# Kernel tuning notes

Hardware: AMD Instinct MI355X
Metric: run time of the kernel (lower is better)

Reference implementation:

```python
import jax, jax.numpy as jnp
import numpy as np

B, T, C = 2, 2048, 1024
H, HD = 16, 64
M = 256  # per memory bank
K_CANON = 4


def setup_inputs() -> dict:
    key = jax.random.key(0)
    ks = jax.random.split(key, 10)
    s = 0.02
    return {
        "x": jax.random.normal(ks[0], (B, T, C), jnp.float32),
        "fwd_mem": jax.random.normal(ks[1], (B, M, C), jnp.float32),
        "rev_mem": jax.random.normal(ks[2], (B, M, C), jnp.float32),
        "Wq": jax.random.normal(ks[3], (C, C), jnp.float32) * s,
        "Wk": jax.random.normal(ks[4], (C, C), jnp.float32) * s,
        "Wv": jax.random.normal(ks[5], (C, C), jnp.float32) * s,
        "Wo": jax.random.normal(ks[6], (C, C), jnp.float32) * s,
        "gate_w": jax.random.normal(ks[7], (H, C), jnp.float32) * s,
        "gate_b": jnp.zeros((H,), jnp.float32),
        "canon_w": jax.random.normal(ks[8], (C, 1, K_CANON), jnp.float32) * s,
        "canon_bias": jax.random.normal(ks[9], (C,), jnp.float32) * s,
    }


def _canon_conv(y, canon_w, canon_bias):
    # causal depthwise conv1d with residual; torch weight [C,1,K] -> WIO kernel [K,1,C]
    kern = jnp.transpose(canon_w, (2, 1, 0))
    y_pad = jnp.pad(y, ((0, 0), (K_CANON - 1, 0), (0, 0)))
    conv = jax.lax.conv_general_dilated(
        y_pad, kern, window_strides=(1,), padding='VALID',
        dimension_numbers=('NWC', 'WIO', 'NWC'), feature_group_count=C)
    return y + conv + canon_bias


def reference(x, fwd_mem, rev_mem, Wq, Wk, Wv, Wo, gate_w, gate_b, canon_w, canon_bias):
    Bn, Tn, Cn = x.shape
    scale = 1.0 / np.sqrt(HD)

    q = x @ Wq.T  # [B,T,C]
    k = x @ Wk.T
    v = x @ Wv.T
    # memory integration: project memories with same k/v proj, concat on seq dim
    k = jnp.concatenate([k, fwd_mem @ Wk.T, rev_mem @ Wk.T], axis=1)  # [B,S,C]
    v = jnp.concatenate([v, fwd_mem @ Wv.T, rev_mem @ Wv.T], axis=1)
    S = k.shape[1]
    mem_len = S - Tn

    def heads(t):
        return t.reshape(Bn, -1, H, HD).transpose(0, 2, 1, 3)  # [B,h,S,hd]

    qh, kh, vh = heads(q), heads(k), heads(v)
    scores = jnp.einsum('bhtd,bhsd->bhts', qh, kh) * scale  # [B,h,T,S]
    # causal mask over the first T key columns; memory columns fully visible
    causal = jnp.triu(jnp.ones((Tn, Tn), bool), k=1)
    full_mask = jnp.pad(causal, ((0, 0), (0, mem_len)))  # [T,S]
    scores = jnp.where(full_mask[None, None], -jnp.inf, scores)
    w = jax.nn.softmax(scores, axis=-1)

    # split chunk vs memory, gate memory contribution per head
    w_chunk, w_mem = w[..., :Tn], w[..., Tn:]
    v_chunk, v_mem = vh[:, :, :Tn], vh[:, :, Tn:]
    Y_chunk = jnp.einsum('bhts,bhsd->bhtd', w_chunk, v_chunk)
    Y_mem = jnp.einsum('bhtm,bhmd->bhtd', w_mem, v_mem)
    g = jax.nn.sigmoid(q @ gate_w.T + gate_b)  # [B,T,h]
    g = g.transpose(0, 2, 1)[..., None]  # [B,h,T,1]
    Y = Y_chunk + g * Y_mem

    attn_out = Y.transpose(0, 2, 1, 3).reshape(Bn, Tn, Cn)
    attn_out = _canon_conv(attn_out, canon_w, canon_bias)
    return attn_out @ Wo.T
```

## Files before the change

### kernel.cpp

```cpp
#include <hip/hip_runtime.h>
#include <hip/hip_bf16.h>
#include <cstdint>


typedef __bf16 bf16x8_t __attribute__((ext_vector_type(8)));
typedef __bf16 bf16x4_t __attribute__((ext_vector_type(4)));
typedef float f32x4_t __attribute__((ext_vector_type(4)));

__device__ __forceinline__ f32x4_t mfma16(bf16x8_t a, bf16x8_t b, f32x4_t c) {
    return __builtin_amdgcn_mfma_f32_16x16x32_bf16(a, b, c, 0, 0, 0);
}

__device__ __forceinline__ void gl2lds16(const void* g, void* l) {
    __builtin_amdgcn_global_load_lds(
        (__attribute__((address_space(1))) uint32_t*)(uintptr_t)g,
        (__attribute__((address_space(3))) uint32_t*)l, 16, 0, 0);
}

#define OFF_X   0
#define OFF_FWD 4194304
#define OFF_REV 4718592
#define OFF_WQ  5242880
#define OFF_WK  6291456
#define OFF_WV  7340032
#define OFF_WO  8388608
#define OFF_GW  9437184
#define OFF_GB  9453568
#define OFF_CW  9453584
#define OFF_CB  9457680
#define N_TOT   9458704

__global__ __launch_bounds__(256) void conv_all_kernel(
    const void* p0, const void* p1, const void* p2, const void* p3,
    const void* p4, const void* p5, const void* p6, const void* p7,
    const void* p8, const void* p9, const void* p10,
    __hip_bfloat16* __restrict__ arena)
{
    const int i = (blockIdx.x * 256 + threadIdx.x) * 4;
    if (i >= N_TOT) return;
    const void* src; int off;
    if      (i < OFF_FWD) { src = p0;  off = OFF_X;   }
    else if (i < OFF_REV) { src = p1;  off = OFF_FWD; }
    else if (i < OFF_WQ)  { src = p2;  off = OFF_REV; }
    else if (i < OFF_WK)  { src = p3;  off = OFF_WQ;  }
    else if (i < OFF_WV)  { src = p4;  off = OFF_WK;  }
    else if (i < OFF_WO)  { src = p5;  off = OFF_WV;  }
    else if (i < OFF_GW)  { src = p6;  off = OFF_WO;  }
    else if (i < OFF_GB)  { src = p7;  off = OFF_GW;  }
    else if (i < OFF_CW)  { src = p8;  off = OFF_GB;  }
    else if (i < OFF_CB)  { src = p9;  off = OFF_CW;  }
    else                  { src = p10; off = OFF_CB;  }
    const int j = i - off;
    const float4 f = *(const float4*)((const float*)src + j);
    arena[i + 0] = __float2bfloat16(f.x);
    arena[i + 1] = __float2bfloat16(f.y);
    arena[i + 2] = __float2bfloat16(f.z);
    arena[i + 3] = __float2bfloat16(f.w);
}

__device__ __forceinline__ void gemm_core(
    const __hip_bfloat16* __restrict__ A, const __hip_bfloat16* __restrict__ B,
    void* __restrict__ C, int ldc, int f32o, int arow0, int brow0,
    __hip_bfloat16* As, __hip_bfloat16* Bs)
{
    const int tid  = threadIdx.x;
    const int lane = tid & 63;
    const int wid  = tid >> 6;
    const int q4   = lane >> 4;
    const int c16  = lane & 15;
    const int wm   = (wid >> 1) * 64;
    const int wn   = (wid & 1) * 64;
    const int c0 = tid;
    const int c1 = tid + 256;
    const __hip_bfloat16* gA0 = A + (size_t)(arow0 + (c0 >> 2)) * 1024 + ((c0 & 3) << 3);
    const __hip_bfloat16* gA1 = A + (size_t)(arow0 + (c1 >> 2)) * 1024 + ((c1 & 3) << 3);
    const __hip_bfloat16* gB0 = B + (size_t)(brow0 + (c0 >> 2)) * 1024 + ((c0 & 3) << 3);
    const __hip_bfloat16* gB1 = B + (size_t)(brow0 + (c1 >> 2)) * 1024 + ((c1 & 3) << 3);

    f32x4_t acc[4][4];
#pragma unroll
    for (int i = 0; i < 4; ++i)
#pragma unroll
        for (int j = 0; j < 4; ++j)
#pragma unroll
            for (int r = 0; r < 4; ++r) acc[i][j][r] = 0.0f;

    gl2lds16(gA0, As + c0 * 8);
    gl2lds16(gA1, As + c1 * 8);
    gl2lds16(gB0, Bs + c0 * 8);
    gl2lds16(gB1, Bs + c1 * 8);

    for (int it = 0; it < 32; ++it) {
        __hip_bfloat16* curA = As + (it & 1) * 4096;
        __hip_bfloat16* curB = Bs + (it & 1) * 4096;
        __syncthreads();
        if (it < 31) {
            const int nk = (it + 1) * 32;
            __hip_bfloat16* nA = As + ((it + 1) & 1) * 4096;
            __hip_bfloat16* nB = Bs + ((it + 1) & 1) * 4096;
            gl2lds16(gA0 + nk, nA + c0 * 8);
            gl2lds16(gA1 + nk, nA + c1 * 8);
            gl2lds16(gB0 + nk, nB + c0 * 8);
            gl2lds16(gB1 + nk, nB + c1 * 8);
        }
        bf16x8_t af[4], bfr[4];
#pragma unroll
        for (int i = 0; i < 4; ++i)
            af[i] = *(const bf16x8_t*)&curA[(wm + i * 16 + c16) * 32 + q4 * 8];
#pragma unroll
        for (int j = 0; j < 4; ++j)
            bfr[j] = *(const bf16x8_t*)&curB[(wn + j * 16 + c16) * 32 + q4 * 8];
#pragma unroll
        for (int i = 0; i < 4; ++i)
#pragma unroll
            for (int j = 0; j < 4; ++j)
                acc[i][j] = mfma16(af[i], bfr[j], acc[i][j]);
    }
#pragma unroll
    for (int i = 0; i < 4; ++i) {
        const int mg = arow0 + wm + i * 16 + q4 * 4;
#pragma unroll
        for (int j = 0; j < 4; ++j) {
            const int ng = brow0 + wn + j * 16 + c16;
#pragma unroll
            for (int r = 0; r < 4; ++r) {
                const size_t idx = (size_t)(mg + r) * ldc + ng;
                if (f32o) ((float*)C)[idx] = acc[i][j][r];
                else ((__hip_bfloat16*)C)[idx] = __float2bfloat16(acc[i][j][r]);
            }
        }
    }
}

__global__ __launch_bounds__(256) void qkv_kernel(
    const __hip_bfloat16* __restrict__ x, const __hip_bfloat16* __restrict__ Wqk,
    const __hip_bfloat16* __restrict__ Wv,
    __hip_bfloat16* __restrict__ QK, __hip_bfloat16* __restrict__ Vt)
{
    __shared__ __align__(16) __hip_bfloat16 As[2 * 128 * 32];
    __shared__ __align__(16) __hip_bfloat16 Bs[2 * 128 * 32];
    int id = blockIdx.x;
    if (id < 640)
        gemm_core(x, Wqk, QK, 2048, 0, (id >> 4) * 128, (id & 15) * 128, As, Bs);
    else {
        id -= 640;
        gemm_core(Wv, x, Vt, 5120, 0, (id & 7) * 128, (id >> 3) * 128, As, Bs);
    }
}

__global__ __launch_bounds__(256) void gemm_bt_kernel(
    const __hip_bfloat16* __restrict__ A, const __hip_bfloat16* __restrict__ B,
    void* __restrict__ C, int ldc, int f32o)
{
    __shared__ __align__(16) __hip_bfloat16 As[2 * 128 * 32];
    __shared__ __align__(16) __hip_bfloat16 Bs[2 * 128 * 32];
    gemm_core(A, B, C, ldc, f32o, blockIdx.x * 128, blockIdx.y * 128, As, Bs);
}

__global__ __launch_bounds__(64) void gate_kernel(
    const __hip_bfloat16* __restrict__ QK, const __hip_bfloat16* __restrict__ gw,
    const __hip_bfloat16* __restrict__ gb, float* __restrict__ G)
{
    const int base = blockIdx.x * 16;
    const int lane = threadIdx.x;
    const int q4   = lane >> 4;
    const int c16  = lane & 15;
    f32x4_t acc = {0.0f, 0.0f, 0.0f, 0.0f};
    const __hip_bfloat16* qrow = QK + (size_t)(base + c16) * 2048 + q4 * 8;
    const __hip_bfloat16* wrow = gw + (size_t)c16 * 1024 + q4 * 8;
#pragma unroll
    for (int kk = 0; kk < 32; ++kk) {
        const bf16x8_t a = *(const bf16x8_t*)(qrow + kk * 32);
        const bf16x8_t w = *(const bf16x8_t*)(wrow + kk * 32);
        acc = mfma16(a, w, acc);
    }
    const float bias = __bfloat162float(gb[c16]);
#pragma unroll
    for (int r = 0; r < 4; ++r) {
        const int row = base + q4 * 4 + r;
        G[(size_t)row * 16 + c16] = 1.0f / (1.0f + __expf(-(acc[r] + bias)));
    }
}

__global__ __launch_bounds__(256, 4) void attn_kernel(
    const __hip_bfloat16* __restrict__ QK,
    const __hip_bfloat16* __restrict__ Vt,
    const float* __restrict__ G, __hip_bfloat16* __restrict__ Y)
{
    __shared__ __align__(16) __hip_bfloat16 Ks[2][64 * 64];
    __shared__ __align__(16) __hip_bfloat16 Vs[64 * 64];
    __shared__ __align__(16) __hip_bfloat16 Plds[4][16 * 64];
    const int flat = blockIdx.x;
    const int bh   = flat & 31;
    const int tIdx = 31 - (flat >> 5);
    const int b    = bh >> 4;
    const int h    = bh & 15;
    const int tid  = threadIdx.x;
    const int wid  = tid >> 6;
    const int lane = tid & 63;
    const int q4   = lane >> 4;
    const int c16  = lane & 15;
    const int rowbase = tIdx * 64 + wid * 16;

    const __hip_bfloat16* qrow = QK + (size_t)(b * 2048 + rowbase + c16) * 2048 + h * 64;
    const bf16x8_t qa0 = *(const bf16x8_t*)(qrow + q4 * 8);
    const bf16x8_t qa1 = *(const bf16x8_t*)(qrow + 32 + q4 * 8);

    float rs[4], gate[4];
    f32x4_t acc[4];
#pragma unroll
    for (int fp = 0; fp < 4; ++fp)
#pragma unroll
        for (int r = 0; r < 4; ++r) acc[fp][r] = 0.0f;
#pragma unroll
    for (int r = 0; r < 4; ++r) {
        rs[r] = 0.0f;
        gate[r] = G[(size_t)(b * 2048 + rowbase + q4 * 4 + r) * 16 + h];
    }

    const int nCausal = tIdx + 1;
    const int nTiles  = nCausal + 8;
    auto kvRow = [&](int tile) -> int {
        if (tile < nCausal) return b * 2048 + tile * 64;
        const int mi = (tile - nCausal) * 64;
        return (mi < 256) ? 4096 + b * 256 + mi : 4608 + b * 256 + (mi - 256);
    };

    const int srow0 = tid >> 3,         sch0 = (tid & 7) ^ (srow0 & 7);
    const int srow1 = (tid + 256) >> 3, sch1 = (tid & 7) ^ (srow1 & 7);
    const int sw0 = (q4 ^ (c16 & 7)) * 8;
    const int sw1 = ((q4 + 4) ^ (c16 & 7)) * 8;
    const __hip_bfloat16* Kbase = QK + 1024 + h * 64;

    {
        const int vr0 = kvRow(0);
        gl2lds16(Kbase + (size_t)(vr0 + srow0) * 2048 + sch0 * 8, &Ks[0][tid * 8]);
        gl2lds16(Kbase + (size_t)(vr0 + srow1) * 2048 + sch1 * 8, &Ks[0][(tid + 256) * 8]);
    }

    const float SCL = 0.18033688f;

    for (int tile = 0; tile < nTiles; ++tile) {
        const int cur = tile & 1;
        const int vr  = kvRow(tile);
        __syncthreads();
        gl2lds16(Vt + (size_t)(h * 64 + srow0) * 5120 + vr + sch0 * 8, &Vs[tid * 8]);
        gl2lds16(Vt + (size_t)(h * 64 + srow1) * 5120 + vr + sch1 * 8, &Vs[(tid + 256) * 8]);
        if (tile + 1 < nTiles) {
            const int nr = kvRow(tile + 1);
            gl2lds16(Kbase + (size_t)(nr + srow0) * 2048 + sch0 * 8, &Ks[cur ^ 1][tid * 8]);
            gl2lds16(Kbase + (size_t)(nr + srow1) * 2048 + sch1 * 8, &Ks[cur ^ 1][(tid + 256) * 8]);
        }
        const bool isMem  = (tile >= nCausal);
        const bool isDiag = (tile == nCausal - 1);
        bf16x8_t kb0[4], kb1[4];
#pragma unroll
        for (int f = 0; f < 4; ++f) {
            kb0[f] = *(const bf16x8_t*)&Ks[cur][(f * 16 + c16) * 64 + sw0];
            kb1[f] = *(const bf16x8_t*)&Ks[cur][(f * 16 + c16) * 64 + sw1];
        }
        f32x4_t sc[4];
#pragma unroll
        for (int f = 0; f < 4; ++f) {
            f32x4_t z = {0.0f, 0.0f, 0.0f, 0.0f};
            z = mfma16(qa0, kb0[f], z);
            z = mfma16(qa1, kb1[f], z);
            sc[f] = z;
        }
#pragma unroll
        for (int f = 0; f < 4; ++f)
#pragma unroll
            for (int r = 0; r < 4; ++r) {
                float p = __builtin_amdgcn_exp2f(sc[f][r] * SCL);
                if (isDiag) {
                    const int sg = f * 16 + c16;
                    if (sg > wid * 16 + q4 * 4 + r) p = 0.0f;
                }
                rs[r] += p;
                if (isMem) p *= gate[r];
                const int prow = q4 * 4 + r;
                const int pcol = f * 16 + c16;
                Plds[wid][prow * 64 + (((pcol >> 3) ^ (prow & 7)) << 3) + (pcol & 7)] =
                    __float2bfloat16(p);
            }
        __syncthreads();
        bf16x8_t vb0[4], vb1[4];
#pragma unroll
        for (int f = 0; f < 4; ++f) {
            vb0[f] = *(const bf16x8_t*)&Vs[(f * 16 + c16) * 64 + sw0];
            vb1[f] = *(const bf16x8_t*)&Vs[(f * 16 + c16) * 64 + sw1];
        }
        const bf16x8_t pa0 = *(const bf16x8_t*)&Plds[wid][c16 * 64 + sw0];
        const bf16x8_t pa1 = *(const bf16x8_t*)&Plds[wid][c16 * 64 + sw1];
#pragma unroll
        for (int fp = 0; fp < 4; ++fp) {
            acc[fp] = mfma16(pa0, vb0[fp], acc[fp]);
            acc[fp] = mfma16(pa1, vb1[fp], acc[fp]);
        }
    }
#pragma unroll
    for (int m = 1; m <= 8; m <<= 1)
#pragma unroll
        for (int r = 0; r < 4; ++r) rs[r] += __shfl_xor(rs[r], m, 64);
    float inv[4];
#pragma unroll
    for (int r = 0; r < 4; ++r) inv[r] = 1.0f / rs[r];
#pragma unroll
    for (int fp = 0; fp < 4; ++fp)
#pragma unroll
        for (int r = 0; r < 4; ++r) {
            const int tg = rowbase + q4 * 4 + r;
            Y[(size_t)(b * 2048 + tg) * 1024 + h * 64 + fp * 16 + c16] =
                __float2bfloat16(acc[fp][r] * inv[r]);
        }
}

__global__ __launch_bounds__(256) void canon_kernel(
    const __hip_bfloat16* __restrict__ Yin, const __hip_bfloat16* __restrict__ cw,
    const __hip_bfloat16* __restrict__ cb, __hip_bfloat16* __restrict__ Yout)
{
    const int idx = (blockIdx.x * 256 + threadIdx.x) * 4;
    const int c = idx & 1023;
    const int t = (idx >> 10) & 2047;
    const bf16x4_t y0 = *(const bf16x4_t*)(Yin + idx);
    const bf16x4_t bb = *(const bf16x4_t*)(cb + c);
    float a[4];
#pragma unroll
    for (int i = 0; i < 4; ++i) a[i] = (float)y0[i] + (float)bb[i];
    const bf16x8_t w01 = *(const bf16x8_t*)(cw + c * 4);
    const bf16x8_t w23 = *(const bf16x8_t*)(cw + c * 4 + 8);
#pragma unroll
    for (int j = 0; j < 4; ++j) {
        if (t - 3 + j >= 0) {
            const bf16x4_t yj = *(const bf16x4_t*)(Yin + idx + (j - 3) * 1024);
            a[0] += (float)yj[0] * (float)w01[j];
            a[1] += (float)yj[1] * (float)w01[4 + j];
            a[2] += (float)yj[2] * (float)w23[j];
            a[3] += (float)yj[3] * (float)w23[4 + j];
        }
    }
    bf16x4_t o;
#pragma unroll
    for (int i = 0; i < 4; ++i) o[i] = (__bf16)a[i];
    *(bf16x4_t*)(Yout + idx) = o;
}

extern "C" void kernel_launch(void* const* d_in, const int* in_sizes, int n_in,
                              void* d_out, int out_size, void* d_ws, size_t ws_size,
                              hipStream_t stream)
{
    char* ws = (char*)d_ws;
    const size_t MB = 1ull << 20;
    if (ws_size < 50 * MB) return;

    __hip_bfloat16* arena = (__hip_bfloat16*)ws;
    __hip_bfloat16* QK    = (__hip_bfloat16*)(ws + 19 * MB);
    __hip_bfloat16* Vt    = (__hip_bfloat16*)(ws + 39 * MB);
    float*          G     = (float*)(ws + 49 * MB);
    __hip_bfloat16* Y1    = (__hip_bfloat16*)ws;
    __hip_bfloat16* Y2    = QK;

    const dim3 blk(256);
    conv_all_kernel<<<dim3((N_TOT / 4 + 255) / 256), blk, 0, stream>>>(
        d_in[0], d_in[1], d_in[2], d_in[3], d_in[4], d_in[5], d_in[6],
        d_in[7], d_in[8], d_in[9], d_in[10], arena);

    const __hip_bfloat16* xB  = arena + OFF_X;
    const __hip_bfloat16* WqB = arena + OFF_WQ;
    const __hip_bfloat16* WvB = arena + OFF_WV;
    const __hip_bfloat16* WoB = arena + OFF_WO;

    qkv_kernel<<<dim3(960), blk, 0, stream>>>(xB, WqB, WvB, QK, Vt);
    gate_kernel<<<dim3(256), dim3(64), 0, stream>>>(QK, arena + OFF_GW, arena + OFF_GB, G);
    attn_kernel<<<dim3(1024), blk, 0, stream>>>(QK, Vt, G, Y1);
    canon_kernel<<<dim3(4096), blk, 0, stream>>>(Y1, arena + OFF_CW, arena + OFF_CB, Y2);
    gemm_bt_kernel<<<dim3(32, 8), blk, 0, stream>>>(Y2, WoB, d_out, 1024, 1);
}
```

Measured before the change: 240.0 us.

## Skip Q projection for memory rows, MFMA row sums, prioritize MFMA waves

```diff
diff --git a/kernel.cpp b/kernel.cpp
--- a/kernel.cpp
+++ b/kernel.cpp
@@ -140,10 +140,13 @@
     __shared__ __align__(16) __hip_bfloat16 As[2 * 128 * 32];
     __shared__ __align__(16) __hip_bfloat16 Bs[2 * 128 * 32];
     int id = blockIdx.x;
-    if (id < 640)
+    if (id < 512)
         gemm_core(x, Wqk, QK, 2048, 0, (id >> 4) * 128, (id & 15) * 128, As, Bs);
-    else {
-        id -= 640;
+    else if (id < 576) {
+        id -= 512;
+        gemm_core(x, Wqk, QK, 2048, 0, (32 + (id >> 3)) * 128, (8 + (id & 7)) * 128, As, Bs);
+    } else {
+        id -= 576;
         gemm_core(Wv, x, Vt, 5120, 0, (id & 7) * 128, (id >> 3) * 128, As, Bs);
     }
 }
@@ -206,17 +209,21 @@
     const bf16x8_t qa0 = *(const bf16x8_t*)(qrow + q4 * 8);
     const bf16x8_t qa1 = *(const bf16x8_t*)(qrow + 32 + q4 * 8);
 
-    float rs[4], gate[4];
+    bf16x8_t ones;
+#pragma unroll
+    for (int i = 0; i < 8; ++i) ones[i] = (__bf16)1.0f;
+
+    float gate[4];
     f32x4_t acc[4];
+    f32x4_t rsC = {0.0f, 0.0f, 0.0f, 0.0f};
+    f32x4_t rsM = {0.0f, 0.0f, 0.0f, 0.0f};
 #pragma unroll
     for (int fp = 0; fp < 4; ++fp)
 #pragma unroll
         for (int r = 0; r < 4; ++r) acc[fp][r] = 0.0f;
 #pragma unroll
-    for (int r = 0; r < 4; ++r) {
-        rs[r] = 0.0f;
+    for (int r = 0; r < 4; ++r)
         gate[r] = G[(size_t)(b * 2048 + rowbase + q4 * 4 + r) * 16 + h];
-    }
 
     const int nCausal = tIdx + 1;
     const int nTiles  = nCausal + 8;
@@ -260,6 +267,7 @@
             kb1[f] = *(const bf16x8_t*)&Ks[cur][(f * 16 + c16) * 64 + sw1];
         }
         f32x4_t sc[4];
+        __builtin_amdgcn_s_setprio(1);
 #pragma unroll
         for (int f = 0; f < 4; ++f) {
             f32x4_t z = {0.0f, 0.0f, 0.0f, 0.0f};
@@ -267,6 +275,7 @@
             z = mfma16(qa1, kb1[f], z);
             sc[f] = z;
         }
+        __builtin_amdgcn_s_setprio(0);
 #pragma unroll
         for (int f = 0; f < 4; ++f)
 #pragma unroll
@@ -276,7 +285,6 @@
                     const int sg = f * 16 + c16;
                     if (sg > wid * 16 + q4 * 4 + r) p = 0.0f;
                 }
-                rs[r] += p;
                 if (isMem) p *= gate[r];
                 const int prow = q4 * 4 + r;
                 const int pcol = f * 16 + c16;
@@ -292,19 +300,26 @@
         }
         const bf16x8_t pa0 = *(const bf16x8_t*)&Plds[wid][c16 * 64 + sw0];
         const bf16x8_t pa1 = *(const bf16x8_t*)&Plds[wid][c16 * 64 + sw1];
+        __builtin_amdgcn_s_setprio(1);
+        if (isMem) {
+            rsM = mfma16(pa0, ones, rsM);
+            rsM = mfma16(pa1, ones, rsM);
+        } else {
+            rsC = mfma16(pa0, ones, rsC);
+            rsC = mfma16(pa1, ones, rsC);
+        }
 #pragma unroll
         for (int fp = 0; fp < 4; ++fp) {
             acc[fp] = mfma16(pa0, vb0[fp], acc[fp]);
             acc[fp] = mfma16(pa1, vb1[fp], acc[fp]);
         }
-    }
-#pragma unroll
-    for (int m = 1; m <= 8; m <<= 1)
-#pragma unroll
-        for (int r = 0; r < 4; ++r) rs[r] += __shfl_xor(rs[r], m, 64);
+        __builtin_amdgcn_s_setprio(0);
+    }
+
     float inv[4];
 #pragma unroll
-    for (int r = 0; r < 4; ++r) inv[r] = 1.0f / rs[r];
+    for (int r = 0; r < 4; ++r)
+        inv[r] = gate[r] / fmaf(gate[r], rsC[r], rsM[r]);
 #pragma unroll
     for (int fp = 0; fp < 4; ++fp)
 #pragma unroll
@@ -370,7 +385,7 @@
     const __hip_bfloat16* WvB = arena + OFF_WV;
     const __hip_bfloat16* WoB = arena + OFF_WO;
 
-    qkv_kernel<<<dim3(960), blk, 0, stream>>>(xB, WqB, WvB, QK, Vt);
+    qkv_kernel<<<dim3(896), blk, 0, stream>>>(xB, WqB, WvB, QK, Vt);
     gate_kernel<<<dim3(256), dim3(64), 0, stream>>>(QK, arena + OFF_GW, arena + OFF_GB, G);
     attn_kernel<<<dim3(1024), blk, 0, stream>>>(QK, Vt, G, Y1);
     canon_kernel<<<dim3(4096), blk, 0, stream>>>(Y1, arena + OFF_CW, arena + OFF_CB, Y2);
```

Measured after the change: 232.9 us. -2.9%, faster.
